# Optimization experiments

Hardware: AMD Instinct MI355X
Metric: run time of the kernel (lower is better)

The kernel has to match this reference:

```python
import jax, jax.numpy as jnp
import numpy as np

N = 100000      # nodes
E = 1600000     # edges (avg degree 16)
IN = 256        # in_dim == num_hidden * num_heads
H = 64          # num_hidden (== num_classes here)
NH = 4          # num_heads
NHEADS_TOTAL = 5  # num_layers*num_heads + 1


def _uniform(k, shape, bound):
    return jax.random.uniform(k, shape, jnp.float32, -bound, bound)


def setup_inputs() -> dict:
    key = jax.random.key(0)
    ks = jax.random.split(key, 12)
    # edge list; ensure every node appears as src (nx symmetric graphs have no isolated rows)
    src = jnp.concatenate([jnp.arange(N, dtype=jnp.int32),
                           jax.random.randint(ks[0], (E - N,), 0, N, jnp.int32)])
    dst = jax.random.randint(ks[1], (E,), 0, N, jnp.int32)
    features = jax.random.normal(ks[2], (N, IN), jnp.float32)
    s_in = 1.0 / np.sqrt(IN)
    s_h = 1.0 / np.sqrt(H)
    # stacked per-head params (all 5 heads share shapes since IN == H*NH)
    W_fc = _uniform(ks[3], (NHEADS_TOTAL, IN, H), s_in)
    b_fc = _uniform(ks[4], (NHEADS_TOTAL, H), s_in)
    w_al = _uniform(ks[5], (NHEADS_TOTAL, H), s_h)
    b_al = _uniform(ks[6], (NHEADS_TOTAL,), s_h)
    w_ar = _uniform(ks[7], (NHEADS_TOTAL, H), s_h)
    b_ar = _uniform(ks[8], (NHEADS_TOTAL,), s_h)
    # residual projection for final head (indim 256 -> num_classes 64)
    W_res = _uniform(ks[9], (IN, H), s_in)
    b_res = _uniform(ks[10], (H,), s_in)
    return {"features": features, "src": src, "dst": dst,
            "W_fc": W_fc, "b_fc": b_fc, "w_al": w_al, "b_al": b_al,
            "w_ar": w_ar, "b_ar": b_ar, "W_res": W_res, "b_res": b_res}


def _one_head(last, src, dst, W, b, wl, bl, wr, br):
    ft = last @ W + b                              # [N, H]
    a1 = ft @ wl + bl                              # [N]  (attn_l)
    a2 = ft @ wr + br                              # [N]  (attn_r)
    a = jax.nn.leaky_relu(a1[dst] + a2[src])       # [E]  per-edge score
    # scipy coo.max(axis=0): per-dst max, implicit zeros included -> clamp at 0; detached in original
    a_max = jnp.maximum(jax.ops.segment_max(a, dst, num_segments=N), 0.0)
    a_max = jax.lax.stop_gradient(a_max)
    ea = jnp.exp(a - a_max[dst])                   # [E]
    a_sum = jax.ops.segment_sum(ea, src, num_segments=N)   # spmm with ones: per-src sum
    attn = ea / a_sum[dst]
    # spmm: out[i] = sum_{edges src=i} attn * ft[dst]
    return jax.ops.segment_sum(attn[:, None] * ft[dst], src, num_segments=N)


def reference(features, src, dst, W_fc, b_fc, w_al, b_al, w_ar, b_ar, W_res, b_res):
    heads = [jax.nn.elu(_one_head(features, src, dst,
                                  W_fc[i], b_fc[i], w_al[i], b_al[i], w_ar[i], b_ar[i]))
             for i in range(NH)]
    last = jnp.concatenate(heads, axis=1)          # [N, H*NH] == [N, 256]
    out = _one_head(last, src, dst, W_fc[NH], b_fc[NH], w_al[NH], b_al[NH], w_ar[NH], b_ar[NH])
    # final head: residual=True with residual_fc (indim != num_classes)
    return jax.nn.elu(last @ W_res + b_res + out)  # [N, 64]
```

## Files before the change

### kernel.cpp

```cpp
#include <hip/hip_runtime.h>

typedef unsigned short ushort_t;
typedef __attribute__((ext_vector_type(8))) short bf16x8;
typedef __attribute__((ext_vector_type(4))) float f32x4;

constexpr int Nn = 100000;
constexpr int Ee = 1600000;

constexpr int NBUCK = 391;
constexpr int BCAP  = 6144;
constexpr int CH3   = 8192;
constexpr int NBLK3 = (Ee + CH3 - 1) / CH3;

constexpr size_t O_ROWPS  = 0;
constexpr size_t O_ROWPD  = 400512;
constexpr size_t O_BOFF   = 801024;
constexpr size_t O_GCUR   = 805120;
constexpr size_t O_CSRDST = 809216;
constexpr size_t O_CSCSRC = 7209216;
constexpr size_t O_FTB1   = 13609216;
constexpr size_t O_FTB2   = 64809216;
constexpr size_t O_LASTB  = 77609216;
constexpr size_t O_EACSR  = 180009216;
constexpr size_t O_M4     = 205609216;
constexpr size_t O_S4     = 207209216;
constexpr size_t O_A14    = 208809216;
constexpr size_t O_A24    = 210409216;
constexpr size_t O_M2     = 212009216;
constexpr size_t O_S2     = 212409728;
constexpr size_t O_A12    = 212810240;
constexpr size_t O_A22    = 213210752;
constexpr size_t O_OUT2   = 213611264;
constexpr size_t O_WT1    = 239211264;
constexpr size_t O_WT2    = 239342336;
constexpr size_t O_WTR    = 239375104;
constexpr size_t O_BUFS   = O_FTB1;
constexpr size_t O_BUFD   = O_FTB1 + (size_t)NBUCK * BCAP * 8;
constexpr size_t O_EAL2   = O_EACSR;

__device__ __forceinline__ ushort_t f2bf(float x) {
    unsigned u = __float_as_uint(x);
    unsigned r = (u + 0x7FFFu + ((u >> 16) & 1u)) >> 16;
    return (ushort_t)r;
}
__device__ __forceinline__ float bf2f(ushort_t x) {
    return __uint_as_float(((unsigned)x) << 16);
}
__device__ __forceinline__ float bflo(unsigned u) { return __uint_as_float(u << 16); }
__device__ __forceinline__ float bfhi(unsigned u) { return __uint_as_float(u & 0xffff0000u); }

__global__ void wcvt_k(const float* __restrict__ Wfc, const float* __restrict__ Wres,
                       ushort_t* __restrict__ Wt1, ushort_t* __restrict__ Wt2,
                       ushort_t* __restrict__ WtR) {
    int g = blockIdx.x * 256 + threadIdx.x;
    if (g < 65536) {
        int c = g >> 8, k = g & 255;
        Wt1[g] = f2bf(Wfc[(size_t)(c >> 6) * 16384 + k * 64 + (c & 63)]);
    } else if (g < 81920) {
        int q = g - 65536;
        int c = q >> 8, k = q & 255;
        Wt2[q] = f2bf(Wfc[4 * 16384 + k * 64 + c]);
    } else {
        int q = g - 81920;
        int c = q >> 8, k = q & 255;
        WtR[q] = f2bf(Wres[k * 64 + c]);
    }
}

__global__ __launch_bounds__(256) void p3_bin_k(const int* __restrict__ src,
                                                const int* __restrict__ dst,
                                                int* __restrict__ gcur,
                                                int2* __restrict__ bufs,
                                                int2* __restrict__ bufd) {
    __shared__ int hs[NBUCK], hd[NBUCK], rs[NBUCK], rd[NBUCK];
    int t = threadIdx.x;
    for (int i = t; i < NBUCK; i += 256) { hs[i] = 0; hd[i] = 0; }
    __syncthreads();
    int e0 = blockIdx.x * CH3;
    int ne = min(CH3, Ee - e0);
    for (int i = t; i < ne; i += 256) {
        atomicAdd(&hs[src[e0 + i] >> 8], 1);
        atomicAdd(&hd[dst[e0 + i] >> 8], 1);
    }
    __syncthreads();
    for (int i = t; i < NBUCK; i += 256) {
        rs[i] = hs[i] ? atomicAdd(&gcur[i], hs[i]) : 0;
        rd[i] = hd[i] ? atomicAdd(&gcur[NBUCK + i], hd[i]) : 0;
        hs[i] = 0; hd[i] = 0;
    }
    __syncthreads();
    for (int i = t; i < ne; i += 256) {
        int s = src[e0 + i], d = dst[e0 + i];
        int bu = s >> 8;
        int pos = rs[bu] + atomicAdd(&hs[bu], 1);
        if (pos < BCAP) bufs[(size_t)bu * BCAP + pos] = make_int2(s, d);
        bu = d >> 8;
        pos = rd[bu] + atomicAdd(&hd[bu], 1);
        if (pos < BCAP) bufd[(size_t)bu * BCAP + pos] = make_int2(d, s);
    }
}

__global__ void p2_scan_k(const int* __restrict__ gcur, int* __restrict__ boff,
                          int* __restrict__ rowps, int* __restrict__ rowpd) {
    __shared__ int sh[512];
    int t = threadIdx.x;
    const int* cnt = gcur + blockIdx.x * NBUCK;
    int* bo = boff + blockIdx.x * 392;
    int v = (t < NBUCK) ? min(cnt[t], BCAP) : 0;
    sh[t] = v;
    __syncthreads();
    for (int o = 1; o < 512; o <<= 1) {
        int x = (t >= o) ? sh[t - o] : 0;
        __syncthreads();
        sh[t] += x;
        __syncthreads();
    }
    if (t < NBUCK) bo[t] = sh[t] - v;
    if (t == NBUCK - 1) {
        bo[NBUCK] = sh[t];
        int* rp = blockIdx.x ? rowpd : rowps;
        rp[Nn] = sh[t];
    }
}

__global__ __launch_bounds__(256) void p4_fill_k(const int* __restrict__ gcur,
                                                 const int* __restrict__ boff,
                                                 const int2* __restrict__ bufs,
                                                 const int2* __restrict__ bufd,
                                                 int* __restrict__ rowps,
                                                 int* __restrict__ rowpd,
                                                 int* __restrict__ csr_dst,
                                                 int* __restrict__ csc_src) {
    __shared__ int cnt[256], lofs[256], sc[256];
    int b = blockIdx.x, st = blockIdx.y;
    const int2* buf = (st ? bufd : bufs) + (size_t)b * BCAP;
    int base = boff[st * 392 + b];
    int total = min(gcur[st * NBUCK + b], BCAP);
    int* rowp = st ? rowpd : rowps;
    int* outv = st ? csc_src : csr_dst;
    int t = threadIdx.x, node0 = b << 8;
    cnt[t] = 0;
    __syncthreads();
    for (int i = t; i < total; i += 256) atomicAdd(&cnt[buf[i].x - node0], 1);
    __syncthreads();
    int v = cnt[t];
    sc[t] = v;
    __syncthreads();
    for (int o = 1; o < 256; o <<= 1) {
        int x = (t >= o) ? sc[t - o] : 0;
        __syncthreads();
        sc[t] += x;
        __syncthreads();
    }
    lofs[t] = sc[t] - v;
    if (node0 + t < Nn) rowp[node0 + t] = base + lofs[t];
    cnt[t] = 0;
    __syncthreads();
    for (int i = t; i < total; i += 256) {
        int2 p = buf[i];
        int k = p.x - node0;
        int r = atomicAdd(&cnt[k], 1);
        outv[base + lofs[k] + r] = p.y;
    }
}

template <int ABF16, int BN, int WGM, int FUSEA, int ADD, int ELU, int BF16OUT>
__global__ __launch_bounds__(256) void mgemm_k(
    const float* __restrict__ Af, const ushort_t* __restrict__ Ab,
    const ushort_t* __restrict__ Bt, const float* __restrict__ bias,
    const float* __restrict__ addp,
    ushort_t* __restrict__ outb, float* __restrict__ outf, int ostride,
    const float* __restrict__ wl, const float* __restrict__ wr,
    const float* __restrict__ blp, const float* __restrict__ brp,
    float* __restrict__ a1, float* __restrict__ a2, int astride) {
    constexpr int MROWS = 128 / WGM;
    constexpr int MREP = MROWS / 16;
    constexpr int LDA = 40;
    __shared__ short As[128 * LDA];
    __shared__ short Bs[BN * LDA];
    int tid = threadIdx.x;
    int m0 = blockIdx.x * 128;
    int col0 = blockIdx.y * BN;
    int w = tid >> 6, l = tid & 63;
    int wr_ = w % WGM, wc = w / WGM;
    int lr = l & 15, lg = l >> 4;
    f32x4 acc[MREP][4];
#pragma unroll
    for (int m = 0; m < MREP; ++m)
#pragma unroll
        for (int n = 0; n < 4; ++n) acc[m][n] = (f32x4){0.f, 0.f, 0.f, 0.f};

    for (int kc = 0; kc < 8; ++kc) {
        int k0 = kc * 32;
        if (ABF16 == 0) {
            int r = tid >> 1, half = tid & 1;
            int grow = m0 + r;
            float4 f0, f1, f2, f3;
            if (grow < Nn) {
                const float4* ap = (const float4*)(Af + (size_t)grow * 256 + k0 + half * 16);
                f0 = ap[0]; f1 = ap[1]; f2 = ap[2]; f3 = ap[3];
            } else {
                f0 = f1 = f2 = f3 = make_float4(0.f, 0.f, 0.f, 0.f);
            }
            bf16x8 s0, s1;
            s0[0] = f2bf(f0.x); s0[1] = f2bf(f0.y); s0[2] = f2bf(f0.z); s0[3] = f2bf(f0.w);
            s0[4] = f2bf(f1.x); s0[5] = f2bf(f1.y); s0[6] = f2bf(f1.z); s0[7] = f2bf(f1.w);
            s1[0] = f2bf(f2.x); s1[1] = f2bf(f2.y); s1[2] = f2bf(f2.z); s1[3] = f2bf(f2.w);
            s1[4] = f2bf(f3.x); s1[5] = f2bf(f3.y); s1[6] = f2bf(f3.z); s1[7] = f2bf(f3.w);
            *(bf16x8*)&As[r * LDA + half * 16] = s0;
            *(bf16x8*)&As[r * LDA + half * 16 + 8] = s1;
        } else {
#pragma unroll
            for (int i = 0; i < 2; ++i) {
                int s = tid + i * 256, r = s >> 2, q = s & 3;
                int grow = m0 + r;
                int4 v = make_int4(0, 0, 0, 0);
                if (grow < Nn) v = *(const int4*)(Ab + (size_t)grow * 256 + k0 + q * 8);
                *(int4*)&As[r * LDA + q * 8] = v;
            }
        }
#pragma unroll
        for (int i = 0; i < BN / 64; ++i) {
            int s = tid + i * 256, c = s >> 2, q = s & 3;
            int4 v = *(const int4*)(Bt + (size_t)(col0 + c) * 256 + k0 + q * 8);
            *(int4*)&Bs[c * LDA + q * 8] = v;
        }
        __syncthreads();
        bf16x8 af[MREP], bfr[4];
#pragma unroll
        for (int m = 0; m < MREP; ++m)
            af[m] = *(const bf16x8*)&As[(wr_ * MROWS + m * 16 + lr) * LDA + lg * 8];
#pragma unroll
        for (int n = 0; n < 4; ++n)
            bfr[n] = *(const bf16x8*)&Bs[(wc * 64 + n * 16 + lr) * LDA + lg * 8];
#pragma unroll
        for (int m = 0; m < MREP; ++m)
#pragma unroll
            for (int n = 0; n < 4; ++n)
                acc[m][n] = __builtin_amdgcn_mfma_f32_16x16x32_bf16(af[m], bfr[n], acc[m][n], 0, 0, 0);
        __syncthreads();
    }

    int coln[4];
    float biasv[4], wlv[4] = {}, wrv[4] = {};
    #pragma unroll
    for (int n = 0; n < 4; ++n) {
        coln[n] = col0 + wc * 64 + n * 16 + lr;
        biasv[n] = bias[coln[n]];
        if (FUSEA) { wlv[n] = wl[coln[n]]; wrv[n] = wr[coln[n]]; }
    }
    int head = (col0 + wc * 64) >> 6;
#pragma unroll
    for (int m = 0; m < MREP; ++m) {
#pragma unroll
        for (int e = 0; e < 4; ++e) {
            int row = m0 + wr_ * MROWS + m * 16 + lg * 4 + e;
            bool ok = row < Nn;
            float vv[4], p1 = 0.f, p2 = 0.f;
#pragma unroll
            for (int n = 0; n < 4; ++n) {
                float v = acc[m][n][e] + biasv[n];
                if (ADD) v += ok ? addp[(size_t)row * 64 + coln[n]] : 0.f;
                if (FUSEA) { p1 += v * wlv[n]; p2 += v * wrv[n]; }
                if (ELU) v = v > 0.f ? v : __expf(v) - 1.f;
                vv[n] = v;
            }
            if (FUSEA) {
#pragma unroll
                for (int o = 1; o < 16; o <<= 1) {
                    p1 += __shfl_xor(p1, o);
                    p2 += __shfl_xor(p2, o);
                }
                if (lr == 0 && ok) {
                    a1[(size_t)row * astride + head] = p1 + blp[head];
                    a2[(size_t)row * astride + head] = p2 + brp[head];
                }
            }
            if (ok) {
#pragma unroll
                for (int n = 0; n < 4; ++n) {
                    if (BF16OUT)
                        outb[(size_t)row * ostride + coln[n]] = f2bf(vv[n]);
                    else
                        outf[(size_t)row * ostride + coln[n]] = vv[n];
                }
            }
        }
    }
}

__global__ __launch_bounds__(256) void maxpass4_k(const int* __restrict__ rowpd,
                                                  const int* __restrict__ cscsrc,
                                                  const float* __restrict__ a1,
                                                  const float* __restrict__ a2,
                                                  float* __restrict__ mmax) {
    int tid = threadIdx.x;
    int node = blockIdx.x * 16 + (tid >> 4);
    if (node >= Nn) return;
    int l16 = tid & 15;
    int slot = l16 >> 2, h = l16 & 3;
    int r0 = rowpd[node], r1 = rowpd[node + 1];
    float a1v = a1[node * 4 + h];
    float m = 0.f;
    for (int i = r0 + slot; i < r1; i += 4) {
        int s = cscsrc[i];
        float v = a1v + a2[s * 4 + h];
        float a = v > 0.f ? v : 0.01f * v;
        m = fmaxf(m, a);
    }
    m = fmaxf(m, __shfl_xor(m, 4));
    m = fmaxf(m, __shfl_xor(m, 8));
    if (slot == 0) mmax[node * 4 + h] = m;
}

__global__ __launch_bounds__(256) void maxpass1_k(const int* __restrict__ rowpd,
                                                  const int* __restrict__ cscsrc,
                                                  const float* __restrict__ a1,
                                                  const float* __restrict__ a2,
                                                  float* __restrict__ mmax) {
    int tid = threadIdx.x;
    int node = blockIdx.x * 16 + (tid >> 4);
    if (node >= Nn) return;
    int slot = tid & 15;
    int r0 = rowpd[node], r1 = rowpd[node + 1];
    float a1v = a1[node];
    float m = 0.f;
    for (int i = r0 + slot; i < r1; i += 16) {
        float v = a1v + a2[cscsrc[i]];
        float a = v > 0.f ? v : 0.01f * v;
        m = fmaxf(m, a);
    }
#pragma unroll
    for (int o = 1; o < 16; o <<= 1) m = fmaxf(m, __shfl_xor(m, o));
    if (slot == 0) mmax[node] = m;
}

__global__ __launch_bounds__(256) void sumpass4_k(const int* __restrict__ rowps,
                                                  const int* __restrict__ csrdst,
                                                  const float* __restrict__ a1,
                                                  const float* __restrict__ a2,
                                                  const float* __restrict__ mmax,
                                                  float* __restrict__ eacsr,
                                                  float* __restrict__ Sinv) {
    int tid = threadIdx.x;
    int node = blockIdx.x * 16 + (tid >> 4);
    if (node >= Nn) return;
    int l16 = tid & 15;
    int slot = l16 >> 2, h = l16 & 3;
    int r0 = rowps[node], r1 = rowps[node + 1];
    float a2v = a2[node * 4 + h];
    float S = 0.f;
    for (int i = r0 + slot; i < r1; i += 4) {
        int d = csrdst[i];
        float v = a1[d * 4 + h] + a2v;
        float a = v > 0.f ? v : 0.01f * v;
        float ea = __expf(a - mmax[d * 4 + h]);
        eacsr[(size_t)i * 4 + h] = ea;
        S += ea;
    }
    S += __shfl_xor(S, 4);
    S += __shfl_xor(S, 8);
    if (slot == 0) Sinv[node * 4 + h] = 1.0f / S;
}

__global__ __launch_bounds__(256) void sumpass1_k(const int* __restrict__ rowps,
                                                  const int* __restrict__ csrdst,
                                                  const float* __restrict__ a1,
                                                  const float* __restrict__ a2,
                                                  const float* __restrict__ mmax,
                                                  float* __restrict__ eacsr,
                                                  float* __restrict__ Sinv) {
    int tid = threadIdx.x;
    int node = blockIdx.x * 16 + (tid >> 4);
    if (node >= Nn) return;
    int slot = tid & 15;
    int r0 = rowps[node], r1 = rowps[node + 1];
    float a2v = a2[node];
    float S = 0.f;
    for (int i = r0 + slot; i < r1; i += 16) {
        int d = csrdst[i];
        float v = a1[d] + a2v;
        float a = v > 0.f ? v : 0.01f * v;
        float ea = __expf(a - mmax[d]);
        eacsr[i] = ea;
        S += ea;
    }
#pragma unroll
    for (int o = 1; o < 16; o <<= 1) S += __shfl_xor(S, o);
    if (slot == 0) Sinv[node] = 1.0f / S;
}

__global__ __launch_bounds__(256) void edgeC4_k(const int* __restrict__ rowp,
                                                const int* __restrict__ cdst,
                                                const float* __restrict__ eacsr,
                                                const float* __restrict__ Sinv4,
                                                const ushort_t* __restrict__ ftb,
                                                ushort_t* __restrict__ lastb) {
    int node = blockIdx.x * 4 + (threadIdx.x >> 6);
    int lane = threadIdx.x & 63;
    if (node >= Nn) return;
    int h = lane >> 4;
    const ushort_t* ftl = ftb + lane * 4;
    int r0 = rowp[node], r1 = rowp[node + 1];
    float ax = 0.f, ay = 0.f, az = 0.f, aw = 0.f;
    int i = r0;
    for (; i + 4 <= r1; i += 4) {
        int d[4];
        float w[4];
        uint2 f[4];
#pragma unroll
        for (int j = 0; j < 4; ++j) d[j] = cdst[i + j];
#pragma unroll
        for (int j = 0; j < 4; ++j) w[j] = eacsr[(size_t)(i + j) * 4 + h];
#pragma unroll
        for (int j = 0; j < 4; ++j) f[j] = *(const uint2*)(ftl + (size_t)d[j] * 256);
#pragma unroll
        for (int j = 0; j < 4; ++j) w[j] *= Sinv4[d[j] * 4 + h];
#pragma unroll
        for (int j = 0; j < 4; ++j) {
            ax += w[j] * bflo(f[j].x);
            ay += w[j] * bfhi(f[j].x);
            az += w[j] * bflo(f[j].y);
            aw += w[j] * bfhi(f[j].y);
        }
    }
    for (; i < r1; ++i) {
        int d = cdst[i];
        float w = eacsr[(size_t)i * 4 + h] * Sinv4[d * 4 + h];
        uint2 f = *(const uint2*)(ftl + (size_t)d * 256);
        ax += w * bflo(f.x);
        ay += w * bfhi(f.x);
        az += w * bflo(f.y);
        aw += w * bfhi(f.y);
    }
    ax = ax > 0.f ? ax : __expf(ax) - 1.f;
    ay = ay > 0.f ? ay : __expf(ay) - 1.f;
    az = az > 0.f ? az : __expf(az) - 1.f;
    aw = aw > 0.f ? aw : __expf(aw) - 1.f;
    uint2 o2;
    o2.x = (unsigned)f2bf(ax) | ((unsigned)f2bf(ay) << 16);
    o2.y = (unsigned)f2bf(az) | ((unsigned)f2bf(aw) << 16);
    *(uint2*)(lastb + (size_t)node * 256 + lane * 4) = o2;
}

__global__ __launch_bounds__(256) void edgeC1_k(const int* __restrict__ rowp,
                                                const int* __restrict__ cdst,
                                                const float* __restrict__ ea,
                                                const float* __restrict__ Sinv2,
                                                const ushort_t* __restrict__ ftb2,
                                                float* __restrict__ outp) {
    int node = blockIdx.x * 4 + (threadIdx.x >> 6);
    int lane = threadIdx.x & 63;
    if (node >= Nn) return;
    int half = lane >> 5, l = lane & 31;
    const ushort_t* ftl = ftb2 + l * 2;
    int r0 = rowp[node], r1 = rowp[node + 1];
    float acc0 = 0.f, acc1 = 0.f;
    int i0 = r0;
    for (; i0 + 8 <= r1; i0 += 8) {
        int d[4];
        float w[4];
        unsigned f[4];
#pragma unroll
        for (int j = 0; j < 4; ++j) {
            int idx = i0 + 2 * j + half;
            d[j] = cdst[idx];
            w[j] = ea[idx];
        }
#pragma unroll
        for (int j = 0; j < 4; ++j) f[j] = *(const unsigned*)(ftl + (size_t)d[j] * 64);
#pragma unroll
        for (int j = 0; j < 4; ++j) w[j] *= Sinv2[d[j]];
#pragma unroll
        for (int j = 0; j < 4; ++j) {
            acc0 += w[j] * bflo(f[j]);
            acc1 += w[j] * bfhi(f[j]);
        }
    }
    for (; i0 < r1; i0 += 2) {
        int i = i0 + half;
        if (i < r1) {
            int d = cdst[i];
            float w = ea[i] * Sinv2[d];
            unsigned f = *(const unsigned*)(ftl + (size_t)d * 64);
            acc0 += w * bflo(f);
            acc1 += w * bfhi(f);
        }
    }
    acc0 += __shfl_xor(acc0, 32);
    acc1 += __shfl_xor(acc1, 32);
    if (lane < 32) {
        *(float2*)(outp + (size_t)node * 64 + l * 2) = make_float2(acc0, acc1);
    }
}

extern "C" void kernel_launch(void* const* d_in, const int* in_sizes, int n_in,
                              void* d_out, int out_size, void* d_ws, size_t ws_size,
                              hipStream_t stream) {
    const float* features = (const float*)d_in[0];
    const int* src = (const int*)d_in[1];
    const int* dst = (const int*)d_in[2];
    const float* W_fc = (const float*)d_in[3];
    const float* b_fc = (const float*)d_in[4];
    const float* w_al = (const float*)d_in[5];
    const float* b_al = (const float*)d_in[6];
    const float* w_ar = (const float*)d_in[7];
    const float* b_ar = (const float*)d_in[8];
    const float* W_res = (const float*)d_in[9];
    const float* b_res = (const float*)d_in[10];
    float* out = (float*)d_out;
    char* ws = (char*)d_ws;

    int* rowps = (int*)(ws + O_ROWPS);
    int* rowpd = (int*)(ws + O_ROWPD);
    int* boff = (int*)(ws + O_BOFF);
    int* gcur = (int*)(ws + O_GCUR);
    int* csr_dst = (int*)(ws + O_CSRDST);
    int* csc_src = (int*)(ws + O_CSCSRC);
    int2* bufs = (int2*)(ws + O_BUFS);
    int2* bufd = (int2*)(ws + O_BUFD);
    ushort_t* ftb1 = (ushort_t*)(ws + O_FTB1);
    ushort_t* ftb2 = (ushort_t*)(ws + O_FTB2);
    ushort_t* lastb = (ushort_t*)(ws + O_LASTB);
    float* eacsr = (float*)(ws + O_EACSR);
    float* m4 = (float*)(ws + O_M4);
    float* S4 = (float*)(ws + O_S4);
    float* a1_4 = (float*)(ws + O_A14);
    float* a2_4 = (float*)(ws + O_A24);
    float* m2 = (float*)(ws + O_M2);
    float* S2 = (float*)(ws + O_S2);
    float* a1_2 = (float*)(ws + O_A12);
    float* a2_2 = (float*)(ws + O_A22);
    float* out2 = (float*)(ws + O_OUT2);
    float* ea_l2 = (float*)(ws + O_EAL2);
    ushort_t* Wt1 = (ushort_t*)(ws + O_WT1);
    ushort_t* Wt2 = (ushort_t*)(ws + O_WT2);
    ushort_t* WtR = (ushort_t*)(ws + O_WTR);

    wcvt_k<<<384, 256, 0, stream>>>(W_fc, W_res, Wt1, Wt2, WtR);

    hipMemsetAsync(gcur, 0, 2 * NBUCK * 4, stream);
    p3_bin_k<<<NBLK3, 256, 0, stream>>>(src, dst, gcur, bufs, bufd);
    p2_scan_k<<<2, 512, 0, stream>>>(gcur, boff, rowps, rowpd);
    p4_fill_k<<<dim3(NBUCK, 2), 256, 0, stream>>>(gcur, boff, bufs, bufd,
                                                  rowps, rowpd, csr_dst, csc_src);

    const int GB = (Nn + 127) / 128;
    const int NW = (Nn + 3) / 4;
    const int NW16 = (Nn + 15) / 16;
    mgemm_k<0, 128, 2, 1, 0, 0, 1><<<dim3(GB, 2), 256, 0, stream>>>(
        features, nullptr, Wt1, b_fc, nullptr,
        ftb1, nullptr, 256, w_al, w_ar, b_al, b_ar, a1_4, a2_4, 4);
    maxpass4_k<<<NW16, 256, 0, stream>>>(rowpd, csc_src, a1_4, a2_4, m4);
    sumpass4_k<<<NW16, 256, 0, stream>>>(rowps, csr_dst, a1_4, a2_4, m4, eacsr, S4);
    edgeC4_k<<<NW, 256, 0, stream>>>(rowps, csr_dst, eacsr, S4, ftb1, lastb);

    mgemm_k<1, 64, 4, 1, 0, 0, 1><<<dim3(GB, 1), 256, 0, stream>>>(
        nullptr, lastb, Wt2, b_fc + 256, nullptr,
        ftb2, nullptr, 64, w_al + 256, w_ar + 256, b_al + 4, b_ar + 4,
        a1_2, a2_2, 1);
    maxpass1_k<<<NW16, 256, 0, stream>>>(rowpd, csc_src, a1_2, a2_2, m2);
    sumpass1_k<<<NW16, 256, 0, stream>>>(rowps, csr_dst, a1_2, a2_2, m2, ea_l2, S2);
    edgeC1_k<<<NW, 256, 0, stream>>>(rowps, csr_dst, ea_l2, S2, ftb2, out2);

    mgemm_k<1, 64, 4, 0, 1, 1, 0><<<dim3(GB, 1), 256, 0, stream>>>(
        nullptr, lastb, WtR, b_res, out2,
        nullptr, out, 64, nullptr, nullptr, nullptr, nullptr, nullptr, nullptr, 0);
}
```

Before: 450.5 us.

## Recompute edge attention weights from packed per-node params instead of storing per-edge exps

The sum pass no longer writes per-edge exponentials. It packs a1, the per-node max and the reciprocal sum into a float4 per node, and the aggregation kernels recompute the leaky-relu and exp score per edge from that gathered record. This removes a large per-edge write and read stream in exchange for extra exp work and a wider random gather per edge. Separately, the first GEMM now covers both 128-column panels in one block, so the A tile is loaded and converted to bf16 only once. The cost is more accumulator registers per thread.

```diff
diff --git a/kernel.cpp b/kernel.cpp
--- a/kernel.cpp
+++ b/kernel.cpp
@@ -21,13 +21,12 @@
 constexpr size_t O_FTB1   = 13609216;
 constexpr size_t O_FTB2   = 64809216;
 constexpr size_t O_LASTB  = 77609216;
-constexpr size_t O_EACSR  = 180009216;
+constexpr size_t O_P4     = 180009216;
+constexpr size_t O_P2     = 196809216;
 constexpr size_t O_M4     = 205609216;
-constexpr size_t O_S4     = 207209216;
 constexpr size_t O_A14    = 208809216;
 constexpr size_t O_A24    = 210409216;
 constexpr size_t O_M2     = 212009216;
-constexpr size_t O_S2     = 212409728;
 constexpr size_t O_A12    = 212810240;
 constexpr size_t O_A22    = 213210752;
 constexpr size_t O_OUT2   = 213611264;
@@ -36,15 +35,11 @@
 constexpr size_t O_WTR    = 239375104;
 constexpr size_t O_BUFS   = O_FTB1;
 constexpr size_t O_BUFD   = O_FTB1 + (size_t)NBUCK * BCAP * 8;
-constexpr size_t O_EAL2   = O_EACSR;
 
 __device__ __forceinline__ ushort_t f2bf(float x) {
     unsigned u = __float_as_uint(x);
     unsigned r = (u + 0x7FFFu + ((u >> 16) & 1u)) >> 16;
     return (ushort_t)r;
-}
-__device__ __forceinline__ float bf2f(ushort_t x) {
-    return __uint_as_float(((unsigned)x) << 16);
 }
 __device__ __forceinline__ float bflo(unsigned u) { return __uint_as_float(u << 16); }
 __device__ __forceinline__ float bfhi(unsigned u) { return __uint_as_float(u & 0xffff0000u); }
@@ -164,7 +159,7 @@
     }
 }
 
-template <int ABF16, int BN, int WGM, int FUSEA, int ADD, int ELU, int BF16OUT>
+template <int ABF16, int BN, int NPAN, int WGM, int FUSEA, int ADD, int ELU, int BF16OUT>
 __global__ __launch_bounds__(256) void mgemm_k(
     const float* __restrict__ Af, const ushort_t* __restrict__ Ab,
     const ushort_t* __restrict__ Bt, const float* __restrict__ bias,
@@ -177,18 +172,20 @@
     constexpr int MREP = MROWS / 16;
     constexpr int LDA = 40;
     __shared__ short As[128 * LDA];
-    __shared__ short Bs[BN * LDA];
+    __shared__ short Bs[NPAN][BN * LDA];
     int tid = threadIdx.x;
     int m0 = blockIdx.x * 128;
-    int col0 = blockIdx.y * BN;
+    int col0 = blockIdx.y * (BN * NPAN);
     int w = tid >> 6, l = tid & 63;
     int wr_ = w % WGM, wc = w / WGM;
     int lr = l & 15, lg = l >> 4;
-    f32x4 acc[MREP][4];
-#pragma unroll
-    for (int m = 0; m < MREP; ++m)
-#pragma unroll
-        for (int n = 0; n < 4; ++n) acc[m][n] = (f32x4){0.f, 0.f, 0.f, 0.f};
+    f32x4 acc[NPAN][MREP][4];
+#pragma unroll
+    for (int p = 0; p < NPAN; ++p)
+#pragma unroll
+        for (int m = 0; m < MREP; ++m)
+#pragma unroll
+            for (int n = 0; n < 4; ++n) acc[p][m][n] = (f32x4){0.f, 0.f, 0.f, 0.f};
 
     for (int kc = 0; kc < 8; ++kc) {
         int k0 = kc * 32;
@@ -220,69 +217,78 @@
             }
         }
 #pragma unroll
-        for (int i = 0; i < BN / 64; ++i) {
-            int s = tid + i * 256, c = s >> 2, q = s & 3;
-            int4 v = *(const int4*)(Bt + (size_t)(col0 + c) * 256 + k0 + q * 8);
-            *(int4*)&Bs[c * LDA + q * 8] = v;
-        }
+        for (int p = 0; p < NPAN; ++p)
+#pragma unroll
+            for (int i = 0; i < BN / 64; ++i) {
+                int s = tid + i * 256, c = s >> 2, q = s & 3;
+                int4 v = *(const int4*)(Bt + (size_t)(col0 + p * BN + c) * 256 + k0 + q * 8);
+                *(int4*)&Bs[p][c * LDA + q * 8] = v;
+            }
         __syncthreads();
-        bf16x8 af[MREP], bfr[4];
+        bf16x8 af[MREP];
 #pragma unroll
         for (int m = 0; m < MREP; ++m)
             af[m] = *(const bf16x8*)&As[(wr_ * MROWS + m * 16 + lr) * LDA + lg * 8];
 #pragma unroll
-        for (int n = 0; n < 4; ++n)
-            bfr[n] = *(const bf16x8*)&Bs[(wc * 64 + n * 16 + lr) * LDA + lg * 8];
-#pragma unroll
-        for (int m = 0; m < MREP; ++m)
+        for (int p = 0; p < NPAN; ++p) {
+            bf16x8 bfr[4];
 #pragma unroll
             for (int n = 0; n < 4; ++n)
-                acc[m][n] = __builtin_amdgcn_mfma_f32_16x16x32_bf16(af[m], bfr[n], acc[m][n], 0, 0, 0);
+                bfr[n] = *(const bf16x8*)&Bs[p][(wc * 64 + n * 16 + lr) * LDA + lg * 8];
+#pragma unroll
+            for (int m = 0; m < MREP; ++m)
+#pragma unroll
+                for (int n = 0; n < 4; ++n)
+                    acc[p][m][n] = __builtin_amdgcn_mfma_f32_16x16x32_bf16(af[m], bfr[n], acc[p][m][n], 0, 0, 0);
+        }
         __syncthreads();
     }
 
-    int coln[4];
-    float biasv[4], wlv[4] = {}, wrv[4] = {};
-    #pragma unroll
-    for (int n = 0; n < 4; ++n) {
-        coln[n] = col0 + wc * 64 + n * 16 + lr;
-        biasv[n] = bias[coln[n]];
-        if (FUSEA) { wlv[n] = wl[coln[n]]; wrv[n] = wr[coln[n]]; }
-    }
-    int head = (col0 + wc * 64) >> 6;
-#pragma unroll
-    for (int m = 0; m < MREP; ++m) {
-#pragma unroll
-        for (int e = 0; e < 4; ++e) {
-            int row = m0 + wr_ * MROWS + m * 16 + lg * 4 + e;
-            bool ok = row < Nn;
-            float vv[4], p1 = 0.f, p2 = 0.f;
-#pragma unroll
-            for (int n = 0; n < 4; ++n) {
-                float v = acc[m][n][e] + biasv[n];
-                if (ADD) v += ok ? addp[(size_t)row * 64 + coln[n]] : 0.f;
-                if (FUSEA) { p1 += v * wlv[n]; p2 += v * wrv[n]; }
-                if (ELU) v = v > 0.f ? v : __expf(v) - 1.f;
-                vv[n] = v;
-            }
-            if (FUSEA) {
-#pragma unroll
-                for (int o = 1; o < 16; o <<= 1) {
-                    p1 += __shfl_xor(p1, o);
-                    p2 += __shfl_xor(p2, o);
+#pragma unroll
+    for (int p = 0; p < NPAN; ++p) {
+        int coln[4];
+        float biasv[4], wlv[4] = {}, wrv[4] = {};
+#pragma unroll
+        for (int n = 0; n < 4; ++n) {
+            coln[n] = col0 + p * BN + wc * 64 + n * 16 + lr;
+            biasv[n] = bias[coln[n]];
+            if (FUSEA) { wlv[n] = wl[coln[n]]; wrv[n] = wr[coln[n]]; }
+        }
+        int head = (col0 + p * BN + wc * 64) >> 6;
+#pragma unroll
+        for (int m = 0; m < MREP; ++m) {
+#pragma unroll
+            for (int e = 0; e < 4; ++e) {
+                int row = m0 + wr_ * MROWS + m * 16 + lg * 4 + e;
+                bool ok = row < Nn;
+                float vv[4], p1 = 0.f, p2 = 0.f;
+#pragma unroll
+                for (int n = 0; n < 4; ++n) {
+                    float v = acc[p][m][n][e] + biasv[n];
+                    if (ADD) v += ok ? addp[(size_t)row * 64 + coln[n]] : 0.f;
+                    if (FUSEA) { p1 += v * wlv[n]; p2 += v * wrv[n]; }
+                    if (ELU) v = v > 0.f ? v : __expf(v) - 1.f;
+                    vv[n] = v;
                 }
-                if (lr == 0 && ok) {
-                    a1[(size_t)row * astride + head] = p1 + blp[head];
-                    a2[(size_t)row * astride + head] = p2 + brp[head];
+                if (FUSEA) {
+#pragma unroll
+                    for (int o = 1; o < 16; o <<= 1) {
+                        p1 += __shfl_xor(p1, o);
+                        p2 += __shfl_xor(p2, o);
+                    }
+                    if (lr == 0 && ok) {
+                        a1[(size_t)row * astride + head] = p1 + blp[head];
+                        a2[(size_t)row * astride + head] = p2 + brp[head];
+                    }
                 }
-            }
-            if (ok) {
-#pragma unroll
-                for (int n = 0; n < 4; ++n) {
-                    if (BF16OUT)
-                        outb[(size_t)row * ostride + coln[n]] = f2bf(vv[n]);
-                    else
-                        outf[(size_t)row * ostride + coln[n]] = vv[n];
+                if (ok) {
+#pragma unroll
+                    for (int n = 0; n < 4; ++n) {
+                        if (BF16OUT)
+                            outb[(size_t)row * ostride + coln[n]] = f2bf(vv[n]);
+                        else
+                            outf[(size_t)row * ostride + coln[n]] = vv[n];
+                    }
                 }
             }
         }
@@ -340,8 +346,7 @@
                                                   const float* __restrict__ a1,
                                                   const float* __restrict__ a2,
                                                   const float* __restrict__ mmax,
-                                                  float* __restrict__ eacsr,
-                                                  float* __restrict__ Sinv) {
+                                                  float4* __restrict__ P4) {
     int tid = threadIdx.x;
     int node = blockIdx.x * 16 + (tid >> 4);
     if (node >= Nn) return;
@@ -354,13 +359,12 @@
         int d = csrdst[i];
         float v = a1[d * 4 + h] + a2v;
         float a = v > 0.f ? v : 0.01f * v;
-        float ea = __expf(a - mmax[d * 4 + h]);
-        eacsr[(size_t)i * 4 + h] = ea;
-        S += ea;
+        S += __expf(a - mmax[d * 4 + h]);
     }
     S += __shfl_xor(S, 4);
     S += __shfl_xor(S, 8);
-    if (slot == 0) Sinv[node * 4 + h] = 1.0f / S;
+    if (slot == 0)
+        P4[node * 4 + h] = make_float4(a1[node * 4 + h], mmax[node * 4 + h], 1.0f / S, 0.f);
 }
 
 __global__ __launch_bounds__(256) void sumpass1_k(const int* __restrict__ rowps,
@@ -368,8 +372,7 @@
                                                   const float* __restrict__ a1,
                                                   const float* __restrict__ a2,
                                                   const float* __restrict__ mmax,
-                                                  float* __restrict__ eacsr,
-                                                  float* __restrict__ Sinv) {
+                                                  float4* __restrict__ P2) {
     int tid = threadIdx.x;
     int node = blockIdx.x * 16 + (tid >> 4);
     if (node >= Nn) return;
@@ -381,41 +384,46 @@
         int d = csrdst[i];
         float v = a1[d] + a2v;
         float a = v > 0.f ? v : 0.01f * v;
-        float ea = __expf(a - mmax[d]);
-        eacsr[i] = ea;
-        S += ea;
+        S += __expf(a - mmax[d]);
     }
 #pragma unroll
     for (int o = 1; o < 16; o <<= 1) S += __shfl_xor(S, o);
-    if (slot == 0) Sinv[node] = 1.0f / S;
+    if (slot == 0)
+        P2[node] = make_float4(a1[node], mmax[node], 1.0f / S, 0.f);
 }
 
 __global__ __launch_bounds__(256) void edgeC4_k(const int* __restrict__ rowp,
                                                 const int* __restrict__ cdst,
-                                                const float* __restrict__ eacsr,
-                                                const float* __restrict__ Sinv4,
+                                                const float4* __restrict__ P4,
+                                                const float* __restrict__ a2,
                                                 const ushort_t* __restrict__ ftb,
                                                 ushort_t* __restrict__ lastb) {
     int node = blockIdx.x * 4 + (threadIdx.x >> 6);
     int lane = threadIdx.x & 63;
     if (node >= Nn) return;
     int h = lane >> 4;
+    float a2v = a2[node * 4 + h];
     const ushort_t* ftl = ftb + lane * 4;
     int r0 = rowp[node], r1 = rowp[node + 1];
     float ax = 0.f, ay = 0.f, az = 0.f, aw = 0.f;
     int i = r0;
     for (; i + 4 <= r1; i += 4) {
         int d[4];
+        uint2 f[4];
+        float4 P[4];
         float w[4];
-        uint2 f[4];
 #pragma unroll
         for (int j = 0; j < 4; ++j) d[j] = cdst[i + j];
 #pragma unroll
-        for (int j = 0; j < 4; ++j) w[j] = eacsr[(size_t)(i + j) * 4 + h];
-#pragma unroll
         for (int j = 0; j < 4; ++j) f[j] = *(const uint2*)(ftl + (size_t)d[j] * 256);
 #pragma unroll
-        for (int j = 0; j < 4; ++j) w[j] *= Sinv4[d[j] * 4 + h];
+        for (int j = 0; j < 4; ++j) P[j] = P4[(size_t)d[j] * 4 + h];
+#pragma unroll
+        for (int j = 0; j < 4; ++j) {
+            float v = P[j].x + a2v;
+            v = v > 0.f ? v : 0.01f * v;
+            w[j] = __expf(v - P[j].y) * P[j].z;
+        }
 #pragma unroll
         for (int j = 0; j < 4; ++j) {
             ax += w[j] * bflo(f[j].x);
@@ -426,8 +434,11 @@
     }
     for (; i < r1; ++i) {
         int d = cdst[i];
-        float w = eacsr[(size_t)i * 4 + h] * Sinv4[d * 4 + h];
         uint2 f = *(const uint2*)(ftl + (size_t)d * 256);
+        float4 P = P4[(size_t)d * 4 + h];
+        float v = P.x + a2v;
+        v = v > 0.f ? v : 0.01f * v;
+        float w = __expf(v - P.y) * P.z;
         ax += w * bflo(f.x);
         ay += w * bfhi(f.x);
         az += w * bflo(f.y);
@@ -445,32 +456,36 @@
 
 __global__ __launch_bounds__(256) void edgeC1_k(const int* __restrict__ rowp,
                                                 const int* __restrict__ cdst,
-                                                const float* __restrict__ ea,
-                                                const float* __restrict__ Sinv2,
+                                                const float4* __restrict__ P2,
+                                                const float* __restrict__ a2,
                                                 const ushort_t* __restrict__ ftb2,
                                                 float* __restrict__ outp) {
     int node = blockIdx.x * 4 + (threadIdx.x >> 6);
     int lane = threadIdx.x & 63;
     if (node >= Nn) return;
     int half = lane >> 5, l = lane & 31;
+    float a2v = a2[node];
     const ushort_t* ftl = ftb2 + l * 2;
     int r0 = rowp[node], r1 = rowp[node + 1];
     float acc0 = 0.f, acc1 = 0.f;
     int i0 = r0;
     for (; i0 + 8 <= r1; i0 += 8) {
         int d[4];
+        unsigned f[4];
+        float4 P[4];
         float w[4];
-        unsigned f[4];
+#pragma unroll
+        for (int j = 0; j < 4; ++j) d[j] = cdst[i0 + 2 * j + half];
+#pragma unroll
+        for (int j = 0; j < 4; ++j) f[j] = *(const unsigned*)(ftl + (size_t)d[j] * 64);
+#pragma unroll
+        for (int j = 0; j < 4; ++j) P[j] = P2[d[j]];
 #pragma unroll
         for (int j = 0; j < 4; ++j) {
-            int idx = i0 + 2 * j + half;
-            d[j] = cdst[idx];
-            w[j] = ea[idx];
-        }
-#pragma unroll
-        for (int j = 0; j < 4; ++j) f[j] = *(const unsigned*)(ftl + (size_t)d[j] * 64);
-#pragma unroll
-        for (int j = 0; j < 4; ++j) w[j] *= Sinv2[d[j]];
+            float v = P[j].x + a2v;
+            v = v > 0.f ? v : 0.01f * v;
+            w[j] = __expf(v - P[j].y) * P[j].z;
+        }
 #pragma unroll
         for (int j = 0; j < 4; ++j) {
             acc0 += w[j] * bflo(f[j]);
@@ -481,8 +496,11 @@
         int i = i0 + half;
         if (i < r1) {
             int d = cdst[i];
-            float w = ea[i] * Sinv2[d];
             unsigned f = *(const unsigned*)(ftl + (size_t)d * 64);
+            float4 P = P2[d];
+            float v = P.x + a2v;
+            v = v > 0.f ? v : 0.01f * v;
+            float w = __expf(v - P.y) * P.z;
             acc0 += w * bflo(f);
             acc1 += w * bfhi(f);
         }
@@ -522,17 +540,15 @@
     ushort_t* ftb1 = (ushort_t*)(ws + O_FTB1);
     ushort_t* ftb2 = (ushort_t*)(ws + O_FTB2);
     ushort_t* lastb = (ushort_t*)(ws + O_LASTB);
-    float* eacsr = (float*)(ws + O_EACSR);
+    float4* P4 = (float4*)(ws + O_P4);
+    float4* P2 = (float4*)(ws + O_P2);
     float* m4 = (float*)(ws + O_M4);
-    float* S4 = (float*)(ws + O_S4);
     float* a1_4 = (float*)(ws + O_A14);
     float* a2_4 = (float*)(ws + O_A24);
     float* m2 = (float*)(ws + O_M2);
-    float* S2 = (float*)(ws + O_S2);
     float* a1_2 = (float*)(ws + O_A12);
     float* a2_2 = (float*)(ws + O_A22);
     float* out2 = (float*)(ws + O_OUT2);
-    float* ea_l2 = (float*)(ws + O_EAL2);
     ushort_t* Wt1 = (ushort_t*)(ws + O_WT1);
     ushort_t* Wt2 = (ushort_t*)(ws + O_WT2);
     ushort_t* WtR = (ushort_t*)(ws + O_WTR);
@@ -548,22 +564,22 @@
     const int GB = (Nn + 127) / 128;
     const int NW = (Nn + 3) / 4;
     const int NW16 = (Nn + 15) / 16;
-    mgemm_k<0, 128, 2, 1, 0, 0, 1><<<dim3(GB, 2), 256, 0, stream>>>(
+    mgemm_k<0, 128, 2, 2, 1, 0, 0, 1><<<dim3(GB, 1), 256, 0, stream>>>(
         features, nullptr, Wt1, b_fc, nullptr,
         ftb1, nullptr, 256, w_al, w_ar, b_al, b_ar, a1_4, a2_4, 4);
     maxpass4_k<<<NW16, 256, 0, stream>>>(rowpd, csc_src, a1_4, a2_4, m4);
-    sumpass4_k<<<NW16, 256, 0, stream>>>(rowps, csr_dst, a1_4, a2_4, m4, eacsr, S4);
-    edgeC4_k<<<NW, 256, 0, stream>>>(rowps, csr_dst, eacsr, S4, ftb1, lastb);
-
-    mgemm_k<1, 64, 4, 1, 0, 0, 1><<<dim3(GB, 1), 256, 0, stream>>>(
+    sumpass4_k<<<NW16, 256, 0, stream>>>(rowps, csr_dst, a1_4, a2_4, m4, P4);
+    edgeC4_k<<<NW, 256, 0, stream>>>(rowps, csr_dst, P4, a2_4, ftb1, lastb);
+
+    mgemm_k<1, 64, 1, 4, 1, 0, 0, 1><<<dim3(GB, 1), 256, 0, stream>>>(
         nullptr, lastb, Wt2, b_fc + 256, nullptr,
         ftb2, nullptr, 64, w_al + 256, w_ar + 256, b_al + 4, b_ar + 4,
         a1_2, a2_2, 1);
     maxpass1_k<<<NW16, 256, 0, stream>>>(rowpd, csc_src, a1_2, a2_2, m2);
-    sumpass1_k<<<NW16, 256, 0, stream>>>(rowps, csr_dst, a1_2, a2_2, m2, ea_l2, S2);
-    edgeC1_k<<<NW, 256, 0, stream>>>(rowps, csr_dst, ea_l2, S2, ftb2, out2);
-
-    mgemm_k<1, 64, 4, 0, 1, 1, 0><<<dim3(GB, 1), 256, 0, stream>>>(
+    sumpass1_k<<<NW16, 256, 0, stream>>>(rowps, csr_dst, a1_2, a2_2, m2, P2);
+    edgeC1_k<<<NW, 256, 0, stream>>>(rowps, csr_dst, P2, a2_2, ftb2, out2);
+
+    mgemm_k<1, 64, 1, 4, 0, 1, 1, 0><<<dim3(GB, 1), 256, 0, stream>>>(
         nullptr, lastb, WtR, b_res, out2,
         nullptr, out, 64, nullptr, nullptr, nullptr, nullptr, nullptr, nullptr, 0);
 }
```

Measured after the change: 486.9 us. 8.1% more time.
